# Optimization experiments

Measured on AMD Instinct MI355X. Metric: run time of the kernel, lower is better.

## Reference

```python
import jax, jax.numpy as jnp
import numpy as np
import math

B, L, D = 2, 2048, 2048
H = 16
HD = D // H  # 128
EPS = 1e-8
ROPE_BASE = 10000.0


def _rms(x, g):
    return x * jax.lax.rsqrt(jnp.mean(x * x, axis=-1, keepdims=True) + EPS) * g


def _rope_tables(seq_len, head_dim, dtype):
    inv_freq = 1.0 / (ROPE_BASE ** (jnp.arange(0, head_dim, 2, dtype=jnp.float32) / head_dim))
    t = jnp.arange(seq_len, dtype=jnp.float32)
    freqs = jnp.outer(t, inv_freq)                 # [L, HD/2]
    emb = jnp.concatenate([freqs, freqs], axis=-1)  # [L, HD]
    return jnp.cos(emb).astype(dtype), jnp.sin(emb).astype(dtype)


def _rotate_half(x):
    x1, x2 = jnp.split(x, 2, axis=-1)
    return jnp.concatenate([-x2, x1], axis=-1)


def setup_inputs() -> dict:
    key = jax.random.key(0)
    ks = jax.random.split(key, 4)
    s = 0.02
    return {
        'x': jax.random.normal(ks[0], (B, L, D), jnp.float32),
        'Wqkv': jax.random.normal(ks[1], (D, 3 * D), jnp.float32) * s,
        'bqkv': jnp.zeros((3 * D,), jnp.float32),
        'Wo': jax.random.normal(ks[2], (D, D), jnp.float32) * s,
        'bo': jnp.zeros((D,), jnp.float32),
        'g1': jnp.ones((D,), jnp.float32),
        'g2': jnp.ones((D,), jnp.float32),
        'Wp': jax.random.normal(ks[3], (D, 8 * D), jnp.float32) * s,
        'bp': jnp.zeros((8 * D,), jnp.float32),
        'Wff_out': jax.random.normal(jax.random.fold_in(key, 7), (4 * D, D), jnp.float32) * s,
        'bff_out': jnp.zeros((D,), jnp.float32),
    }


def reference(x, Wqkv, bqkv, Wo, bo, g1, g2, Wp, bp, Wff_out, bff_out):
    b, l, d = x.shape
    # pre-norm + fused QKV projection
    h = _rms(x, g1)
    qkv = h @ Wqkv + bqkv                                  # [B, L, 3D]
    q, k, v = jnp.split(qkv, 3, axis=-1)
    def heads(t):
        return t.reshape(b, l, H, HD).transpose(0, 2, 1, 3)  # [B, H, L, HD]
    q, k, v = heads(q), heads(k), heads(v)
    # RoPE
    cos, sin = _rope_tables(l, HD, x.dtype)                 # [L, HD]
    cos = cos[None, None]
    sin = sin[None, None]
    q = q * cos + _rotate_half(q) * sin
    k = k * cos + _rotate_half(k) * sin
    # causal SDPA
    scale = 1.0 / math.sqrt(HD)
    scores = jnp.einsum('bhqd,bhkd->bhqk', q, k) * scale
    causal = jnp.tril(jnp.ones((l, l), dtype=bool))
    scores = jnp.where(causal[None, None], scores, jnp.finfo(scores.dtype).min)
    attn = jax.nn.softmax(scores, axis=-1)
    o = jnp.einsum('bhqk,bhkd->bhqd', attn, v)              # [B, H, L, HD]
    o = o.transpose(0, 2, 1, 3).reshape(b, l, d)
    attn_out = o @ Wo + bo
    x = x + attn_out                                        # residual (dropout=0, eval)
    # SwiGLU FFN, pre-norm
    h2 = _rms(x, g2)
    p = h2 @ Wp + bp                                        # [B, L, 8D]
    gate, value = jnp.split(p, 2, axis=-1)
    ff = (jax.nn.silu(gate) * value) @ Wff_out + bff_out
    return x + ff
```

## Files before the change

### kernel.cpp

```cpp
#include <hip/hip_runtime.h>
#include <stdint.h>

typedef unsigned short u16;
typedef float floatx4 __attribute__((ext_vector_type(4)));
typedef short bf16x8 __attribute__((ext_vector_type(8)));

#define DEVI __device__ __forceinline__

#define B_ 2
#define L_ 2048
#define D_ 2048
#define H_ 16
#define HD_ 128
#define M_ 4096

DEVI u16 f2bf(float f) {
  union { float f; uint32_t u; } v; v.f = f;
  uint32_t r = v.u + 0x7fffu + ((v.u >> 16) & 1u);
  return (u16)(r >> 16);
}
DEVI float bf2f(u16 h) {
  union { uint32_t u; float f; } v; v.u = ((uint32_t)h) << 16;
  return v.f;
}

DEVI floatx4 mfma16(bf16x8 a, bf16x8 b, floatx4 c) {
  return __builtin_amdgcn_mfma_f32_16x16x32_bf16(a, b, c, 0, 0, 0);
}

DEVI void gl2lds16(const u16* g, u16* l) {
  __builtin_amdgcn_global_load_lds((const __attribute__((address_space(1))) void*)g,
                                   (__attribute__((address_space(3))) void*)l, 16, 0, 0);
}

__global__ void rmsnorm_kernel(const float* __restrict__ x, const float* __restrict__ g,
                               u16* __restrict__ out) {
  int row = blockIdx.x;
  int tid = threadIdx.x;
  const float* xr = x + (size_t)row * D_;
  float4 v0 = ((const float4*)xr)[tid];
  float4 v1 = ((const float4*)xr)[256 + tid];
  float ss = v0.x*v0.x + v0.y*v0.y + v0.z*v0.z + v0.w*v0.w
           + v1.x*v1.x + v1.y*v1.y + v1.z*v1.z + v1.w*v1.w;
  #pragma unroll
  for (int off = 32; off > 0; off >>= 1) ss += __shfl_xor(ss, off, 64);
  __shared__ float red[4];
  int wv = tid >> 6, ln = tid & 63;
  if (ln == 0) red[wv] = ss;
  __syncthreads();
  float tot = red[0] + red[1] + red[2] + red[3];
  float scale = rsqrtf(tot * (1.0f / (float)D_) + 1e-8f);
  float4 g0 = ((const float4*)g)[tid];
  float4 g1v = ((const float4*)g)[256 + tid];
  u16* orow = out + (size_t)row * D_;
  ushort4 o0, o1;
  o0.x = f2bf(v0.x * scale * g0.x);  o0.y = f2bf(v0.y * scale * g0.y);
  o0.z = f2bf(v0.z * scale * g0.z);  o0.w = f2bf(v0.w * scale * g0.w);
  o1.x = f2bf(v1.x * scale * g1v.x); o1.y = f2bf(v1.y * scale * g1v.y);
  o1.z = f2bf(v1.z * scale * g1v.z); o1.w = f2bf(v1.w * scale * g1v.w);
  ((ushort4*)orow)[tid] = o0;
  ((ushort4*)orow)[256 + tid] = o1;
}

__global__ void transpose_w_kernel(const float* __restrict__ W, u16* __restrict__ Wt,
                                   int Kd, int Nd) {
  __shared__ float tile[32][33];
  int n0 = blockIdx.x * 32, k0 = blockIdx.y * 32;
  int tid = threadIdx.x;
  int r = tid >> 3, c4 = (tid & 7) * 4;
  float4 v = *(const float4*)(W + (size_t)(k0 + r) * Nd + n0 + c4);
  tile[r][c4 + 0] = v.x; tile[r][c4 + 1] = v.y; tile[r][c4 + 2] = v.z; tile[r][c4 + 3] = v.w;
  __syncthreads();
  ushort4 o;
  o.x = f2bf(tile[c4 + 0][r]); o.y = f2bf(tile[c4 + 1][r]);
  o.z = f2bf(tile[c4 + 2][r]); o.w = f2bf(tile[c4 + 3][r]);
  *(ushort4*)(Wt + (size_t)(n0 + r) * Kd + k0 + c4) = o;
}

__global__ void rope_qk_kernel(const u16* __restrict__ qkv, u16* __restrict__ q_r,
                               u16* __restrict__ k_r) {
  int idx = blockIdx.x * 256 + threadIdx.x;
  int i = idx & 63;
  int h = (idx >> 6) & (H_ - 1);
  int l = (idx >> 10) & (L_ - 1);
  int b = idx >> 21;
  float freq = expf(-(float)i * 0.14391156831212787f);
  float ang = (float)l * freq;
  float s, c;
  sincosf(ang, &s, &c);
  size_t base_in = (size_t)(b * L_ + l) * (3 * D_);
  size_t qi = base_in + h * HD_ + i;
  size_t ki = base_in + D_ + h * HD_ + i;
  float q1 = bf2f(qkv[qi]), q2 = bf2f(qkv[qi + 64]);
  float k1 = bf2f(qkv[ki]), k2 = bf2f(qkv[ki + 64]);
  size_t base_out = ((size_t)(b * H_ + h) * L_ + l) * HD_ + i;
  q_r[base_out]      = f2bf(q1 * c - q2 * s);
  q_r[base_out + 64] = f2bf(q2 * c + q1 * s);
  k_r[base_out]      = f2bf(k1 * c - k2 * s);
  k_r[base_out + 64] = f2bf(k2 * c + k1 * s);
}

__global__ void v_transpose_kernel(const u16* __restrict__ qkv, u16* __restrict__ vt) {
  __shared__ u16 tile[32][36];
  int bh = blockIdx.z;
  int d0 = blockIdx.y * 32;
  int l0 = blockIdx.x * 32;
  int b = bh >> 4, h = bh & 15;
  int tid = threadIdx.x;
  int r = tid >> 3, c4 = (tid & 7) * 4;
  const u16* src = qkv + (size_t)(b * L_ + l0 + r) * (3 * D_) + 2 * D_ + h * HD_ + d0 + c4;
  ushort4 v = *(const ushort4*)src;
  tile[r][c4 + 0] = v.x; tile[r][c4 + 1] = v.y; tile[r][c4 + 2] = v.z; tile[r][c4 + 3] = v.w;
  __syncthreads();
  ushort4 o;
  o.x = tile[c4 + 0][r]; o.y = tile[c4 + 1][r]; o.z = tile[c4 + 2][r]; o.w = tile[c4 + 3][r];
  *(ushort4*)(vt + ((size_t)bh * HD_ + d0 + r) * L_ + l0 + c4) = o;
}

template <int MODE>
__launch_bounds__(256, 3)
__global__ void gemm_bt_kernel(const u16* __restrict__ A, const u16* __restrict__ Bt,
                               const float* __restrict__ bias,
                               const float* __restrict__ resid, const u16* __restrict__ gate,
                               void* __restrict__ out, int Nn, int Kk) {
  __shared__ __attribute__((aligned(16))) u16 As[128 * 32];
  __shared__ __attribute__((aligned(16))) u16 Bs[128 * 32];
  int tid = threadIdx.x;
  int wave = tid >> 6, lane = tid & 63, quad = lane >> 4, lr = lane & 15;
  int m0 = blockIdx.y * 128, n0 = blockIdx.x * 128;
  int wm = (wave >> 1) * 64, wn = (wave & 1) * 64;
  floatx4 acc[4][4];
  floatx4 z4 = {0.f, 0.f, 0.f, 0.f};
  #pragma unroll
  for (int i = 0; i < 4; i++)
    #pragma unroll
    for (int j = 0; j < 4; j++) acc[i][j] = z4;
  int drow = tid >> 2;
  int dcol = ((tid & 3) ^ ((drow >> 1) & 3)) * 8;
  const u16* Ap = A + (size_t)m0 * Kk;
  const u16* Bp = Bt + (size_t)n0 * Kk;
  int sw = (quad ^ ((lr >> 1) & 3)) * 8;
  for (int kt = 0; kt < Kk; kt += 32) {
    __syncthreads();
    gl2lds16(Ap + (size_t)drow * Kk + kt + dcol,        As + tid * 8);
    gl2lds16(Ap + (size_t)(drow + 64) * Kk + kt + dcol, As + 2048 + tid * 8);
    gl2lds16(Bp + (size_t)drow * Kk + kt + dcol,        Bs + tid * 8);
    gl2lds16(Bp + (size_t)(drow + 64) * Kk + kt + dcol, Bs + 2048 + tid * 8);
    __syncthreads();
    bf16x8 af[4], bfr[4];
    #pragma unroll
    for (int i = 0; i < 4; i++)
      af[i] = *(const bf16x8*)&As[(wm + i * 16 + lr) * 32 + sw];
    #pragma unroll
    for (int i = 0; i < 4; i++)
      bfr[i] = *(const bf16x8*)&Bs[(wn + i * 16 + lr) * 32 + sw];
    #pragma unroll
    for (int mi = 0; mi < 4; mi++)
      #pragma unroll
      for (int ni = 0; ni < 4; ni++)
        acc[mi][ni] = mfma16(af[mi], bfr[ni], acc[mi][ni]);
  }
  #pragma unroll
  for (int mi = 0; mi < 4; mi++) {
    #pragma unroll
    for (int ni = 0; ni < 4; ni++) {
      int col = n0 + wn + ni * 16 + lr;
      float bcol = bias[col];
      #pragma unroll
      for (int r2 = 0; r2 < 4; r2++) {
        int row = m0 + wm + mi * 16 + quad * 4 + r2;
        float v = acc[mi][ni][r2] + bcol;
        size_t off = (size_t)row * Nn + col;
        if (MODE == 0) {
          ((u16*)out)[off] = f2bf(v);
        } else if (MODE == 1) {
          ((float*)out)[off] = v + resid[off];
        } else {
          float gv = bf2f(gate[off]);
          float sg = gv / (1.f + __expf(-gv));
          ((u16*)out)[off] = f2bf(sg * v);
        }
      }
    }
  }
}

__launch_bounds__(256, 2)
__global__ void attn_kernel(const u16* __restrict__ q_r, const u16* __restrict__ k_r,
                            const u16* __restrict__ vt, u16* __restrict__ o) {
  __shared__ __attribute__((aligned(16))) u16 KPs[128 * 128];
  __shared__ __attribute__((aligned(16))) u16 Vs[128 * 128];
  int bh = blockIdx.y, b = bh >> 4, h = bh & 15;
  int qt = (blockIdx.y < 16) ? blockIdx.x : (15 - blockIdx.x);
  int q0 = qt * 128;
  int tid = threadIdx.x, wave = tid >> 6, lane = tid & 63, quad = lane >> 4, lr = lane & 15;
  int wq0 = wave * 32;
  const u16* Qp = q_r + (size_t)bh * L_ * HD_;
  const u16* Kp = k_r + (size_t)bh * L_ * HD_;
  const u16* Vtp = vt + (size_t)bh * HD_ * L_;
  const float scale = 0.08838834764831845f;
  bf16x8 qf[2][4];
  #pragma unroll
  for (int mi = 0; mi < 2; mi++)
    #pragma unroll
    for (int kk = 0; kk < 4; kk++)
      qf[mi][kk] = *(const bf16x8*)(Qp + (size_t)(q0 + wq0 + mi * 16 + lr) * HD_ + kk * 32 + quad * 8);
  float mrun[2][4], lrun[2][4];
  floatx4 z4 = {0.f, 0.f, 0.f, 0.f};
  floatx4 oacc[2][8];
  #pragma unroll
  for (int mi = 0; mi < 2; mi++) {
    #pragma unroll
    for (int r2 = 0; r2 < 4; r2++) { mrun[mi][r2] = -__builtin_inff(); lrun[mi][r2] = 0.f; }
    #pragma unroll
    for (int di = 0; di < 8; di++) oacc[mi][di] = z4;
  }
  int dr = tid >> 4;
  int dgo = ((tid & 15) ^ dr) * 8;
  for (int jt = 0; jt <= qt; ++jt) {
    __syncthreads();
    #pragma unroll
    for (int p = 0; p < 8; ++p) {
      int r = p * 16 + dr;
      gl2lds16(Kp + (size_t)(jt * 128 + r) * HD_ + dgo, KPs + p * 2048 + tid * 8);
      gl2lds16(Vtp + (size_t)r * L_ + jt * 128 + dgo,   Vs + p * 2048 + tid * 8);
    }
    __syncthreads();
    floatx4 sacc[2][8];
    #pragma unroll
    for (int mi = 0; mi < 2; mi++)
      #pragma unroll
      for (int ni = 0; ni < 8; ni++) sacc[mi][ni] = z4;
    #pragma unroll
    for (int kk = 0; kk < 4; ++kk) {
      bf16x8 kf[8];
      #pragma unroll
      for (int ni = 0; ni < 8; ++ni)
        kf[ni] = *(const bf16x8*)&KPs[(ni * 16 + lr) * 128 + ((kk * 4 + quad) ^ lr) * 8];
      #pragma unroll
      for (int mi = 0; mi < 2; mi++)
        #pragma unroll
        for (int ni = 0; ni < 8; ni++)
          sacc[mi][ni] = mfma16(qf[mi][kk], kf[ni], sacc[mi][ni]);
    }
    __syncthreads();
    bool diag = (jt == qt);
    #pragma unroll
    for (int mi = 0; mi < 2; mi++) {
      #pragma unroll
      for (int r2 = 0; r2 < 4; r2++) {
        int row_abs = q0 + wq0 + mi * 16 + quad * 4 + r2;
        int prow = wq0 + mi * 16 + quad * 4 + r2;
        float sv[8];
        float mloc = -__builtin_inff();
        #pragma unroll
        for (int ni = 0; ni < 8; ni++) {
          float v = sacc[mi][ni][r2] * scale;
          if (diag && (jt * 128 + ni * 16 + lr) > row_abs) v = -__builtin_inff();
          sv[ni] = v;
          mloc = fmaxf(mloc, v);
        }
        #pragma unroll
        for (int off = 1; off < 16; off <<= 1) mloc = fmaxf(mloc, __shfl_xor(mloc, off, 16));
        float mold = mrun[mi][r2];
        float mnew = fmaxf(mold, mloc);
        float alpha = __expf(mold - mnew);
        float ls = 0.f;
        #pragma unroll
        for (int ni = 0; ni < 8; ni++) {
          float p = __expf(sv[ni] - mnew);
          ls += p;
          int slot = (ni * 2 + (lr >> 3)) ^ (prow & 15);
          KPs[prow * 128 + slot * 8 + (lr & 7)] = f2bf(p);
        }
        #pragma unroll
        for (int off = 1; off < 16; off <<= 1) ls += __shfl_xor(ls, off, 16);
        lrun[mi][r2] = lrun[mi][r2] * alpha + ls;
        mrun[mi][r2] = mnew;
        #pragma unroll
        for (int di = 0; di < 8; di++) oacc[mi][di][r2] *= alpha;
      }
    }
    #pragma unroll
    for (int kk = 0; kk < 4; ++kk) {
      bf16x8 pf[2], vf[8];
      #pragma unroll
      for (int mi = 0; mi < 2; mi++)
        pf[mi] = *(const bf16x8*)&KPs[(wq0 + mi * 16 + lr) * 128 + ((kk * 4 + quad) ^ lr) * 8];
      #pragma unroll
      for (int di = 0; di < 8; di++)
        vf[di] = *(const bf16x8*)&Vs[(di * 16 + lr) * 128 + ((kk * 4 + quad) ^ lr) * 8];
      #pragma unroll
      for (int mi = 0; mi < 2; mi++)
        #pragma unroll
        for (int di = 0; di < 8; di++)
          oacc[mi][di] = mfma16(pf[mi], vf[di], oacc[mi][di]);
    }
  }
  #pragma unroll
  for (int mi = 0; mi < 2; mi++) {
    #pragma unroll
    for (int r2 = 0; r2 < 4; r2++) {
      float inv = 1.f / lrun[mi][r2];
      int l_abs = q0 + wq0 + mi * 16 + quad * 4 + r2;
      size_t base = (size_t)(b * L_ + l_abs) * D_ + h * HD_;
      #pragma unroll
      for (int di = 0; di < 8; di++)
        o[base + di * 16 + lr] = f2bf(oacc[mi][di][r2] * inv);
    }
  }
}

extern "C" void kernel_launch(void* const* d_in, const int* in_sizes, int n_in,
                              void* d_out, int out_size, void* d_ws, size_t ws_size,
                              hipStream_t stream) {
  const float* x    = (const float*)d_in[0];
  const float* Wqkv = (const float*)d_in[1];
  const float* bqkv = (const float*)d_in[2];
  const float* Wo   = (const float*)d_in[3];
  const float* bo   = (const float*)d_in[4];
  const float* g1   = (const float*)d_in[5];
  const float* g2   = (const float*)d_in[6];
  const float* Wp   = (const float*)d_in[7];
  const float* bp   = (const float*)d_in[8];
  const float* Wff  = (const float*)d_in[9];
  const float* bff  = (const float*)d_in[10];
  char* ws = (char*)d_ws;
  u16*  wbuf = (u16*)(ws);
  u16*  hbuf = (u16*)(ws + 67108864);
  float* x1  = (float*)(ws + 83886080);
  char* rA = ws + 117440512;
  u16* qkv  = (u16*)(rA);
  u16* q_r  = (u16*)(rA + 50331648);
  u16* k_r  = (u16*)(rA + 67108864);
  u16* vtb  = (u16*)(rA + 83886080);
  u16* ob   = (u16*)(rA + 100663296);
  u16* gate = (u16*)(rA);
  u16* ffin = (u16*)(rA + 67108864);
  float* outp = (float*)d_out;
  dim3 blk(256);

  rmsnorm_kernel<<<M_, blk, 0, stream>>>(x, g1, hbuf);
  transpose_w_kernel<<<dim3(6144 / 32, 2048 / 32), blk, 0, stream>>>(Wqkv, wbuf, 2048, 6144);
  gemm_bt_kernel<0><<<dim3(48, 32), blk, 0, stream>>>(hbuf, wbuf, bqkv, nullptr, nullptr, qkv, 6144, 2048);
  rope_qk_kernel<<<(B_ * L_ * H_ * 64) / 256, blk, 0, stream>>>(qkv, q_r, k_r);
  v_transpose_kernel<<<dim3(L_ / 32, HD_ / 32, B_ * H_), blk, 0, stream>>>(qkv, vtb);
  attn_kernel<<<dim3(L_ / 128, B_ * H_), blk, 0, stream>>>(q_r, k_r, vtb, ob);
  transpose_w_kernel<<<dim3(2048 / 32, 2048 / 32), blk, 0, stream>>>(Wo, wbuf, 2048, 2048);
  gemm_bt_kernel<1><<<dim3(16, 32), blk, 0, stream>>>(ob, wbuf, bo, x, nullptr, x1, 2048, 2048);
  rmsnorm_kernel<<<M_, blk, 0, stream>>>(x1, g2, hbuf);
  transpose_w_kernel<<<dim3(16384 / 32, 2048 / 32), blk, 0, stream>>>(Wp, wbuf, 2048, 16384);
  gemm_bt_kernel<0><<<dim3(64, 32), blk, 0, stream>>>(hbuf, wbuf, bp, nullptr, nullptr, gate, 8192, 2048);
  gemm_bt_kernel<2><<<dim3(64, 32), blk, 0, stream>>>(hbuf, wbuf + (size_t)8192 * 2048, bp + 8192,
                                                      nullptr, gate, ffin, 8192, 2048);
  transpose_w_kernel<<<dim3(2048 / 32, 8192 / 32), blk, 0, stream>>>(Wff, wbuf, 8192, 2048);
  gemm_bt_kernel<1><<<dim3(16, 32), blk, 0, stream>>>(ffin, wbuf, bff, x1, nullptr, outp, 2048, 8192);
}
```

Baseline: 1.208 ms.

## Fuse gate and value FFN GEMMs and deepen GEMM K-tile to 64

After: 1.068 ms. 11.6% less time.

```diff
diff --git a/kernel.cpp b/kernel.cpp
--- a/kernel.cpp
+++ b/kernel.cpp
@@ -117,14 +117,15 @@
   *(ushort4*)(vt + ((size_t)bh * HD_ + d0 + r) * L_ + l0 + c4) = o;
 }
 
+
 template <int MODE>
 __launch_bounds__(256, 3)
 __global__ void gemm_bt_kernel(const u16* __restrict__ A, const u16* __restrict__ Bt,
                                const float* __restrict__ bias,
-                               const float* __restrict__ resid, const u16* __restrict__ gate,
+                               const float* __restrict__ resid,
                                void* __restrict__ out, int Nn, int Kk) {
-  __shared__ __attribute__((aligned(16))) u16 As[128 * 32];
-  __shared__ __attribute__((aligned(16))) u16 Bs[128 * 32];
+  __shared__ __attribute__((aligned(16))) u16 As[128 * 64];
+  __shared__ __attribute__((aligned(16))) u16 Bs[128 * 64];
   int tid = threadIdx.x;
   int wave = tid >> 6, lane = tid & 63, quad = lane >> 4, lr = lane & 15;
   int m0 = blockIdx.y * 128, n0 = blockIdx.x * 128;
@@ -135,30 +136,35 @@
   for (int i = 0; i < 4; i++)
     #pragma unroll
     for (int j = 0; j < 4; j++) acc[i][j] = z4;
-  int drow = tid >> 2;
-  int dcol = ((tid & 3) ^ ((drow >> 1) & 3)) * 8;
+  int dr8 = tid >> 3;
+  int dg = ((tid & 7) ^ (dr8 & 7)) * 8;
   const u16* Ap = A + (size_t)m0 * Kk;
   const u16* Bp = Bt + (size_t)n0 * Kk;
-  int sw = (quad ^ ((lr >> 1) & 3)) * 8;
-  for (int kt = 0; kt < Kk; kt += 32) {
-    __syncthreads();
-    gl2lds16(Ap + (size_t)drow * Kk + kt + dcol,        As + tid * 8);
-    gl2lds16(Ap + (size_t)(drow + 64) * Kk + kt + dcol, As + 2048 + tid * 8);
-    gl2lds16(Bp + (size_t)drow * Kk + kt + dcol,        Bs + tid * 8);
-    gl2lds16(Bp + (size_t)(drow + 64) * Kk + kt + dcol, Bs + 2048 + tid * 8);
-    __syncthreads();
-    bf16x8 af[4], bfr[4];
-    #pragma unroll
-    for (int i = 0; i < 4; i++)
-      af[i] = *(const bf16x8*)&As[(wm + i * 16 + lr) * 32 + sw];
-    #pragma unroll
-    for (int i = 0; i < 4; i++)
-      bfr[i] = *(const bf16x8*)&Bs[(wn + i * 16 + lr) * 32 + sw];
-    #pragma unroll
-    for (int mi = 0; mi < 4; mi++)
-      #pragma unroll
-      for (int ni = 0; ni < 4; ni++)
-        acc[mi][ni] = mfma16(af[mi], bfr[ni], acc[mi][ni]);
+  for (int kt = 0; kt < Kk; kt += 64) {
+    __syncthreads();
+    #pragma unroll
+    for (int p = 0; p < 4; p++)
+      gl2lds16(Ap + (size_t)(p * 32 + dr8) * Kk + kt + dg, As + p * 2048 + tid * 8);
+    #pragma unroll
+    for (int p = 0; p < 4; p++)
+      gl2lds16(Bp + (size_t)(p * 32 + dr8) * Kk + kt + dg, Bs + p * 2048 + tid * 8);
+    __syncthreads();
+    #pragma unroll
+    for (int kk = 0; kk < 2; ++kk) {
+      int swz = ((kk * 4 + quad) ^ (lr & 7)) * 8;
+      bf16x8 af[4], bfr[4];
+      #pragma unroll
+      for (int i = 0; i < 4; i++)
+        af[i] = *(const bf16x8*)&As[(wm + i * 16 + lr) * 64 + swz];
+      #pragma unroll
+      for (int i = 0; i < 4; i++)
+        bfr[i] = *(const bf16x8*)&Bs[(wn + i * 16 + lr) * 64 + swz];
+      #pragma unroll
+      for (int mi = 0; mi < 4; mi++)
+        #pragma unroll
+        for (int ni = 0; ni < 4; ni++)
+          acc[mi][ni] = mfma16(af[mi], bfr[ni], acc[mi][ni]);
+    }
   }
   #pragma unroll
   for (int mi = 0; mi < 4; mi++) {
@@ -173,13 +179,80 @@
         size_t off = (size_t)row * Nn + col;
         if (MODE == 0) {
           ((u16*)out)[off] = f2bf(v);
-        } else if (MODE == 1) {
+        } else {
           ((float*)out)[off] = v + resid[off];
-        } else {
-          float gv = bf2f(gate[off]);
-          float sg = gv / (1.f + __expf(-gv));
-          ((u16*)out)[off] = f2bf(sg * v);
         }
+      }
+    }
+  }
+}
+
+__launch_bounds__(256, 2)
+__global__ void ffn_gemm_kernel(const u16* __restrict__ A, const u16* __restrict__ Wt,
+                                const float* __restrict__ bp,
+                                u16* __restrict__ out, int Kk) {
+  __shared__ __attribute__((aligned(16))) u16 As[128 * 64];
+  __shared__ __attribute__((aligned(16))) u16 Bg[128 * 64];
+  __shared__ __attribute__((aligned(16))) u16 Bv[128 * 64];
+  int tid = threadIdx.x;
+  int wave = tid >> 6, lane = tid & 63, quad = lane >> 4, lr = lane & 15;
+  int m0 = blockIdx.y * 128, n0 = blockIdx.x * 128;
+  int wm = (wave >> 1) * 64, wn = (wave & 1) * 64;
+  floatx4 accg[4][4], accv[4][4];
+  floatx4 z4 = {0.f, 0.f, 0.f, 0.f};
+  #pragma unroll
+  for (int i = 0; i < 4; i++)
+    #pragma unroll
+    for (int j = 0; j < 4; j++) { accg[i][j] = z4; accv[i][j] = z4; }
+  int dr8 = tid >> 3;
+  int dg = ((tid & 7) ^ (dr8 & 7)) * 8;
+  const u16* Ap = A + (size_t)m0 * Kk;
+  const u16* Bgp = Wt + (size_t)n0 * Kk;
+  const u16* Bvp = Wt + (size_t)(8192 + n0) * Kk;
+  for (int kt = 0; kt < Kk; kt += 64) {
+    __syncthreads();
+    #pragma unroll
+    for (int p = 0; p < 4; p++)
+      gl2lds16(Ap + (size_t)(p * 32 + dr8) * Kk + kt + dg, As + p * 2048 + tid * 8);
+    #pragma unroll
+    for (int p = 0; p < 4; p++)
+      gl2lds16(Bgp + (size_t)(p * 32 + dr8) * Kk + kt + dg, Bg + p * 2048 + tid * 8);
+    #pragma unroll
+    for (int p = 0; p < 4; p++)
+      gl2lds16(Bvp + (size_t)(p * 32 + dr8) * Kk + kt + dg, Bv + p * 2048 + tid * 8);
+    __syncthreads();
+    #pragma unroll
+    for (int kk = 0; kk < 2; ++kk) {
+      int swz = ((kk * 4 + quad) ^ (lr & 7)) * 8;
+      bf16x8 af[4], bgf[4], bvf[4];
+      #pragma unroll
+      for (int i = 0; i < 4; i++) {
+        af[i]  = *(const bf16x8*)&As[(wm + i * 16 + lr) * 64 + swz];
+        bgf[i] = *(const bf16x8*)&Bg[(wn + i * 16 + lr) * 64 + swz];
+        bvf[i] = *(const bf16x8*)&Bv[(wn + i * 16 + lr) * 64 + swz];
+      }
+      #pragma unroll
+      for (int mi = 0; mi < 4; mi++)
+        #pragma unroll
+        for (int ni = 0; ni < 4; ni++) {
+          accg[mi][ni] = mfma16(af[mi], bgf[ni], accg[mi][ni]);
+          accv[mi][ni] = mfma16(af[mi], bvf[ni], accv[mi][ni]);
+        }
+    }
+  }
+  #pragma unroll
+  for (int mi = 0; mi < 4; mi++) {
+    #pragma unroll
+    for (int ni = 0; ni < 4; ni++) {
+      int col = n0 + wn + ni * 16 + lr;
+      float bg = bp[col], bv = bp[col + 8192];
+      #pragma unroll
+      for (int r2 = 0; r2 < 4; r2++) {
+        int row = m0 + wm + mi * 16 + quad * 4 + r2;
+        float gv = accg[mi][ni][r2] + bg;
+        float vv = accv[mi][ni][r2] + bv;
+        float sg = gv / (1.f + __expf(-gv));
+        out[(size_t)row * 8192 + col] = f2bf(sg * vv);
       }
     }
   }
@@ -335,24 +408,21 @@
   u16* k_r  = (u16*)(rA + 67108864);
   u16* vtb  = (u16*)(rA + 83886080);
   u16* ob   = (u16*)(rA + 100663296);
-  u16* gate = (u16*)(rA);
-  u16* ffin = (u16*)(rA + 67108864);
+  u16* ffin = (u16*)(rA);
   float* outp = (float*)d_out;
   dim3 blk(256);
 
   rmsnorm_kernel<<<M_, blk, 0, stream>>>(x, g1, hbuf);
   transpose_w_kernel<<<dim3(6144 / 32, 2048 / 32), blk, 0, stream>>>(Wqkv, wbuf, 2048, 6144);
-  gemm_bt_kernel<0><<<dim3(48, 32), blk, 0, stream>>>(hbuf, wbuf, bqkv, nullptr, nullptr, qkv, 6144, 2048);
+  gemm_bt_kernel<0><<<dim3(48, 32), blk, 0, stream>>>(hbuf, wbuf, bqkv, nullptr, qkv, 6144, 2048);
   rope_qk_kernel<<<(B_ * L_ * H_ * 64) / 256, blk, 0, stream>>>(qkv, q_r, k_r);
   v_transpose_kernel<<<dim3(L_ / 32, HD_ / 32, B_ * H_), blk, 0, stream>>>(qkv, vtb);
   attn_kernel<<<dim3(L_ / 128, B_ * H_), blk, 0, stream>>>(q_r, k_r, vtb, ob);
   transpose_w_kernel<<<dim3(2048 / 32, 2048 / 32), blk, 0, stream>>>(Wo, wbuf, 2048, 2048);
-  gemm_bt_kernel<1><<<dim3(16, 32), blk, 0, stream>>>(ob, wbuf, bo, x, nullptr, x1, 2048, 2048);
+  gemm_bt_kernel<1><<<dim3(16, 32), blk, 0, stream>>>(ob, wbuf, bo, x, x1, 2048, 2048);
   rmsnorm_kernel<<<M_, blk, 0, stream>>>(x1, g2, hbuf);
   transpose_w_kernel<<<dim3(16384 / 32, 2048 / 32), blk, 0, stream>>>(Wp, wbuf, 2048, 16384);
-  gemm_bt_kernel<0><<<dim3(64, 32), blk, 0, stream>>>(hbuf, wbuf, bp, nullptr, nullptr, gate, 8192, 2048);
-  gemm_bt_kernel<2><<<dim3(64, 32), blk, 0, stream>>>(hbuf, wbuf + (size_t)8192 * 2048, bp + 8192,
-                                                      nullptr, gate, ffin, 8192, 2048);
+  ffn_gemm_kernel<<<dim3(64, 32), blk, 0, stream>>>(hbuf, wbuf, bp, ffin, 2048);
   transpose_w_kernel<<<dim3(2048 / 32, 8192 / 32), blk, 0, stream>>>(Wff, wbuf, 8192, 2048);
-  gemm_bt_kernel<1><<<dim3(16, 32), blk, 0, stream>>>(ffin, wbuf, bff, x1, nullptr, outp, 2048, 8192);
-}
+  gemm_bt_kernel<1><<<dim3(16, 32), blk, 0, stream>>>(ffin, wbuf, bff, x1, outp, 2048, 8192);
+}
```
